# Kernel optimization log

Hardware: AMD Instinct MI355X
Metric: run time of the kernel (lower is better)

## Reference

```python
import jax, jax.numpy as jnp
import numpy as np

U = 512  # units

def hard_sigmoid(x):
    # Keras hard_sigmoid: clip(0.2*x + 0.5, 0, 1)
    return jnp.clip(0.2 * x + 0.5, 0.0, 1.0)

def setup_inputs() -> dict:
    key = jax.random.key(0)
    ks = jax.random.split(key, 9)
    B, T, A, D = 64, 2048, 512, 512  # batch, annotation steps, annotation units, input dim
    s = lambda k, shape, scale: jax.random.normal(k, shape, jnp.float32) * scale
    return {
        "inputs": s(ks[0], (B, D), 1.0),
        "h": s(ks[1], (B, U), 1.0),
        "c": s(ks[2], (B, U), 1.0),
        "annotations": s(ks[3], (B, T, A), 1.0),
        "kernel": s(ks[4], (D + A, 4 * U), 0.02),
        "recurrent_kernel": s(ks[5], (U, 4 * U), 0.02),
        "bias": jnp.zeros((6 * U,), jnp.float32).at[U:2 * U].set(1.0),  # unit_forget_bias
        "kernel_u": s(ks[6], (A, U), 0.02),
        "kernel_w": s(ks[7], (U, U), 0.02),
        "kernel_v": s(ks[8], (U,), 0.02),
    }

def reference(inputs, h, c, annotations, kernel, recurrent_kernel, bias, kernel_u, kernel_w, kernel_v):
    bias_u = bias[4 * U:5 * U]
    # precomputed annotation projection (done once in build()): [B,T,U]
    uh = jnp.einsum('bta,au->btu', annotations, kernel_u) + bias_u
    # Bahdanau attention scores
    Wxstm = h @ kernel_w                                   # [B,U]
    et = jnp.einsum('btu,u->bt', jnp.tanh(uh + Wxstm[:, None, :]), kernel_v)
    at = jax.nn.softmax(et, axis=1)                        # exp/sum in source == softmax
    context = jnp.einsum('bt,bta->ba', at, annotations)    # [B,A]
    x = jnp.concatenate([inputs, context], axis=-1)        # [B, D+A]
    z = x @ kernel + h @ recurrent_kernel + bias[:4 * U]   # [B,4U]
    i = hard_sigmoid(z[:, :U])
    f = hard_sigmoid(z[:, U:2 * U])
    c_new = f * c + i * jnp.tanh(z[:, 2 * U:3 * U])
    o = hard_sigmoid(z[:, 3 * U:])
    h_new = o * jnp.tanh(c_new)
    return h_new
```

## Files before the change

### kernel.cpp

```cpp
#include <hip/hip_runtime.h>

constexpr int U = 512;
constexpr int B = 64;
constexpr int T = 2048;
constexpr int A = 512;

typedef __attribute__((ext_vector_type(8))) short short8;
typedef __attribute__((ext_vector_type(4))) float f32x4;

__device__ __forceinline__ unsigned short f32_to_bf16(float f) {
    unsigned int b = __float_as_uint(f);
    unsigned int r = (b + 0x7FFFu + ((b >> 16) & 1u)) >> 16;
    return (unsigned short)r;
}

__device__ __forceinline__ float bf16_to_f32(short s) {
    return __uint_as_float(((unsigned int)(unsigned short)s) << 16);
}

__device__ __forceinline__ float fast_tanh(float x) {
    float e = exp2f(x * 2.885390081777927f);
    return (e - 1.0f) * __builtin_amdgcn_rcpf(e + 1.0f);
}

__device__ __forceinline__ float hard_sigmoid(float z) {
    return fminf(fmaxf(0.2f * z + 0.5f, 0.0f), 1.0f);
}

__global__ __launch_bounds__(256) void k_prep_s(const float* __restrict__ h,
                                                const float* __restrict__ kw,
                                                float* __restrict__ Sp) {
    int b = blockIdx.x >> 2;
    int kc = blockIdx.x & 3;
    int u = threadIdx.x;
    const float* hb = h + b * U + kc * 128;
    const float* kwb = kw + (size_t)kc * 128 * U;
    float a0 = 0.f, a1 = 0.f;
#pragma unroll 4
    for (int k = 0; k < 128; ++k) {
        float hv = hb[k];
        a0 += hv * kwb[(size_t)k * U + u];
        a1 += hv * kwb[(size_t)k * U + u + 256];
    }
    float* p = Sp + ((size_t)kc * 64 + b) * U;
    p[u] = a0;
    p[u + 256] = a1;
}

__global__ __launch_bounds__(256) void k_s_reduce(const float* __restrict__ Sp,
                                                  const float* __restrict__ bias,
                                                  float* __restrict__ S) {
    int gid = blockIdx.x * 256 + threadIdx.x;
    int b = gid >> 9, u = gid & 511;
    float s = bias[4 * U + u];
#pragma unroll
    for (int kc = 0; kc < 4; ++kc) s += Sp[((size_t)kc * 64 + b) * U + u];
    S[gid] = s;
}

__global__ __launch_bounds__(256) void k_prep_kut(const float* __restrict__ ku,
                                                  unsigned short* __restrict__ kut) {
    __shared__ float tile[32][33];
    int a0 = (blockIdx.x >> 4) << 5;
    int u0 = (blockIdx.x & 15) << 5;
    int c = threadIdx.x & 31, r0 = threadIdx.x >> 5;
#pragma unroll
    for (int p = 0; p < 4; ++p) {
        int r = r0 + p * 8;
        tile[r][c] = ku[(a0 + r) * U + u0 + c];
    }
    __syncthreads();
#pragma unroll
    for (int p = 0; p < 4; ++p) {
        int r = r0 + p * 8;
        kut[(u0 + r) * A + a0 + c] = f32_to_bf16(tile[c][r]);
    }
}

__global__ __launch_bounds__(256) void k_prep_wt(const float* __restrict__ kern,
                                                 const float* __restrict__ rk,
                                                 unsigned short* __restrict__ Wt) {
    __shared__ float tile[32][33];
    int k0 = blockIdx.x << 5;
    int j0 = blockIdx.y << 5;
    int c = threadIdx.x & 31, r0 = threadIdx.x >> 5;
#pragma unroll
    for (int p = 0; p < 4; ++p) {
        int r = r0 + p * 8;
        int k = k0 + r;
        float val = (k < 1024) ? kern[k * 2048 + j0 + c]
                               : rk[(k - 1024) * 2048 + j0 + c];
        tile[r][c] = val;
    }
    __syncthreads();
#pragma unroll
    for (int p = 0; p < 4; ++p) {
        int r = r0 + p * 8;
        Wt[(size_t)(j0 + r) * 1536 + k0 + c] = f32_to_bf16(tile[c][r]);
    }
}

__global__ __launch_bounds__(256, 2) void k_gemm_et(const float* __restrict__ ann,
                                                    const unsigned short* __restrict__ kut,
                                                    const float* __restrict__ S,
                                                    const float* __restrict__ v,
                                                    unsigned short* __restrict__ annb,
                                                    float* __restrict__ etp) {
    __shared__ unsigned short As[128 * 64];
    __shared__ unsigned short Bs[256 * 64];
    __shared__ float red[4][64];

    const int tid = threadIdx.x;
    const int wave = tid >> 6;
    const int lane = tid & 63;
    const int lanelo = lane & 15;
    const int quad = lane >> 4;
    const int wm = wave >> 1, wn = wave & 1;

    const int bid = blockIdx.x;
    const int nt = (bid >> 3) & 1;
    const int mt = (bid & 7) | ((bid >> 4) << 3);
    const int b = mt >> 4;
    const float* aBase = ann + (size_t)mt * 128 * A;
    const unsigned short* bBase = kut + (size_t)nt * 256 * A;
    unsigned short* abOut = annb + (size_t)mt * 128 * A;

    f32x4 acc[4][8];
#pragma unroll
    for (int i = 0; i < 4; ++i)
#pragma unroll
        for (int j = 0; j < 8; ++j) acc[i][j] = {0.f, 0.f, 0.f, 0.f};

    for (int k0 = 0; k0 < A; k0 += 64) {
#pragma unroll
        for (int p = 0; p < 8; ++p) {
            int seg = p * 4 + wave;
            int flat = seg * 1024 + lane * 16;
            int row = flat >> 7;
            int sc = (flat >> 4) & 7;
            int d = sc ^ (row & 7);
            __builtin_amdgcn_global_load_lds(
                (const __attribute__((address_space(1))) void*)(bBase + (size_t)row * A + k0 + d * 8),
                (__attribute__((address_space(3))) void*)((char*)Bs + seg * 1024),
                16, 0, 0);
        }
#pragma unroll
        for (int p = 0; p < 4; ++p) {
            int flat8 = p * 256 + tid;
            int row = flat8 >> 3;
            int c8 = flat8 & 7;
            const float* src = aBase + (size_t)row * A + k0 + c8 * 8;
            f32x4 v0 = *(const f32x4*)src;
            f32x4 v1 = *(const f32x4*)(src + 4);
            short8 pk;
            pk[0] = (short)f32_to_bf16(v0.x);
            pk[1] = (short)f32_to_bf16(v0.y);
            pk[2] = (short)f32_to_bf16(v0.z);
            pk[3] = (short)f32_to_bf16(v0.w);
            pk[4] = (short)f32_to_bf16(v1.x);
            pk[5] = (short)f32_to_bf16(v1.y);
            pk[6] = (short)f32_to_bf16(v1.z);
            pk[7] = (short)f32_to_bf16(v1.w);
            *(short8*)&As[row * 64 + ((c8 ^ (row & 7)) * 8)] = pk;
            if (nt == 0)
                *(short8*)(abOut + (size_t)row * A + k0 + c8 * 8) = pk;
        }
        __syncthreads();
#pragma unroll
        for (int s = 0; s < 2; ++s) {
            int c = s * 4 + quad;
            short8 af[4];
#pragma unroll
            for (int mi = 0; mi < 4; ++mi) {
                int row = wm * 64 + mi * 16 + lanelo;
                af[mi] = *(const short8*)&As[row * 64 + ((c ^ (row & 7)) * 8)];
            }
            short8 bfr[8];
#pragma unroll
            for (int ni = 0; ni < 8; ++ni) {
                int rowb = wn * 128 + ni * 16 + lanelo;
                bfr[ni] = *(const short8*)&Bs[rowb * 64 + ((c ^ (rowb & 7)) * 8)];
            }
#pragma unroll
            for (int mi = 0; mi < 4; ++mi)
#pragma unroll
                for (int ni = 0; ni < 8; ++ni)
                    acc[mi][ni] = __builtin_amdgcn_mfma_f32_16x16x32_bf16(
                        af[mi], bfr[ni], acc[mi][ni], 0, 0, 0);
        }
        __syncthreads();
    }

    float rows[16];
#pragma unroll
    for (int i = 0; i < 16; ++i) rows[i] = 0.f;
#pragma unroll
    for (int ni = 0; ni < 8; ++ni) {
        int n = nt * 256 + wn * 128 + ni * 16 + lanelo;
        float sv = S[b * U + n];
        float vv = v[n];
#pragma unroll
        for (int mi = 0; mi < 4; ++mi)
#pragma unroll
            for (int r = 0; r < 4; ++r)
                rows[mi * 4 + r] += fast_tanh(acc[mi][ni][r] + sv) * vv;
    }
#pragma unroll
    for (int i = 0; i < 16; ++i) {
        rows[i] += __shfl_xor(rows[i], 1);
        rows[i] += __shfl_xor(rows[i], 2);
        rows[i] += __shfl_xor(rows[i], 4);
        rows[i] += __shfl_xor(rows[i], 8);
    }
    if (lanelo == 0) {
#pragma unroll
        for (int mi = 0; mi < 4; ++mi)
#pragma unroll
            for (int r = 0; r < 4; ++r)
                red[wave][mi * 16 + quad * 4 + r] = rows[mi * 4 + r];
    }
    __syncthreads();
    if (tid < 128) {
        int wmv = tid >> 6, ml = tid & 63;
        float sum = red[wmv * 2][ml] + red[wmv * 2 + 1][ml];
        etp[(size_t)nt * (1024 * 128) + (size_t)mt * 128 + tid] = sum;
    }
}

__global__ __launch_bounds__(256) void k_softmax(const float* __restrict__ etp,
                                                 float* __restrict__ at) {
    __shared__ float sred[256];
    int b = blockIdx.x;
    const float* e = etp + b * T;
    float vals[8];
    float mx = -1e30f;
#pragma unroll
    for (int i = 0; i < 8; ++i) {
        int t = threadIdx.x + i * 256;
        float x = e[t] + e[131072 + t];
        vals[i] = x;
        mx = fmaxf(mx, x);
    }
    sred[threadIdx.x] = mx;
    __syncthreads();
    for (int s = 128; s > 0; s >>= 1) {
        if (threadIdx.x < s) sred[threadIdx.x] = fmaxf(sred[threadIdx.x], sred[threadIdx.x + s]);
        __syncthreads();
    }
    mx = sred[0];
    __syncthreads();
    float sum = 0.f;
#pragma unroll
    for (int i = 0; i < 8; ++i) {
        float x = exp2f((vals[i] - mx) * 1.4426950408889634f);
        vals[i] = x;
        sum += x;
    }
    sred[threadIdx.x] = sum;
    __syncthreads();
    for (int s = 128; s > 0; s >>= 1) {
        if (threadIdx.x < s) sred[threadIdx.x] += sred[threadIdx.x + s];
        __syncthreads();
    }
    float inv = 1.0f / sred[0];
#pragma unroll
    for (int i = 0; i < 8; ++i) at[b * T + threadIdx.x + i * 256] = vals[i] * inv;
}

__global__ __launch_bounds__(256) void k_ctx_part(const float* __restrict__ at,
                                                  const unsigned short* __restrict__ annb,
                                                  float* __restrict__ part) {
    __shared__ float buf[4][512];
    int b = blockIdx.x >> 3;
    int tc = blockIdx.x & 7;
    int wave = threadIdx.x >> 6;
    int lane = threadIdx.x & 63;
    const unsigned short* ab = annb + ((size_t)b * T + tc * 256) * A + lane * 8;
    const float* atb = at + b * T + tc * 256;
    float acc[8];
#pragma unroll
    for (int i = 0; i < 8; ++i) acc[i] = 0.f;
    for (int t = wave; t < 256; t += 4) {
        float w = atb[t];
        short8 rv = *(const short8*)(ab + (size_t)t * A);
#pragma unroll
        for (int i = 0; i < 8; ++i) acc[i] += w * bf16_to_f32(rv[i]);
    }
#pragma unroll
    for (int i = 0; i < 8; ++i) buf[wave][lane * 8 + i] = acc[i];
    __syncthreads();
    int a2 = threadIdx.x << 1;
    float s0 = buf[0][a2] + buf[1][a2] + buf[2][a2] + buf[3][a2];
    float s1 = buf[0][a2 + 1] + buf[1][a2 + 1] + buf[2][a2 + 1] + buf[3][a2 + 1];
    float* p = part + ((size_t)b * 8 + tc) * A;
    p[a2] = s0;
    p[a2 + 1] = s1;
}

__global__ __launch_bounds__(256) void k_ctx_reduce(const float* __restrict__ part,
                                                    float* __restrict__ ctx) {
    int b = blockIdx.x;
    for (int a = threadIdx.x; a < A; a += 256) {
        float s = 0.f;
#pragma unroll
        for (int c = 0; c < 8; ++c) s += part[((size_t)b * 8 + c) * A + a];
        ctx[b * A + a] = s;
    }
}

__global__ __launch_bounds__(256) void k_prep_xb(const float* __restrict__ inputs,
                                                 const float* __restrict__ ctx,
                                                 const float* __restrict__ h,
                                                 unsigned short* __restrict__ xb) {
    int b = blockIdx.y;
    int k = blockIdx.x * 256 + threadIdx.x;
    float val;
    if (k < 512) val = inputs[b * 512 + k];
    else if (k < 1024) val = ctx[b * 512 + (k - 512)];
    else val = h[b * 512 + (k - 1024)];
    xb[b * 1536 + k] = f32_to_bf16(val);
}

__global__ __launch_bounds__(256) void k_zgemm(const unsigned short* __restrict__ xb,
                                               const unsigned short* __restrict__ Wt,
                                               float* __restrict__ zpart) {
    const int kc = blockIdx.x & 7;
    const int nt = blockIdx.x >> 3;
    const int wave = threadIdx.x >> 6;
    const int lane = threadIdx.x & 63;
    const int lanelo = lane & 15;
    const int quad = lane >> 4;

    const int n = nt * 64 + wave * 16 + lanelo;
    const unsigned short* bp = Wt + (size_t)n * 1536 + kc * 192 + quad * 8;
    const unsigned short* ap = xb + (size_t)lanelo * 1536 + kc * 192 + quad * 8;

    f32x4 acc[4];
#pragma unroll
    for (int i = 0; i < 4; ++i) acc[i] = {0.f, 0.f, 0.f, 0.f};

#pragma unroll
    for (int ks = 0; ks < 6; ++ks) {
        short8 bfrag = *(const short8*)(bp + ks * 32);
#pragma unroll
        for (int mi = 0; mi < 4; ++mi) {
            short8 afrag = *(const short8*)(ap + (size_t)mi * 16 * 1536 + ks * 32);
            acc[mi] = __builtin_amdgcn_mfma_f32_16x16x32_bf16(afrag, bfrag, acc[mi], 0, 0, 0);
        }
    }

    float* p = zpart + (size_t)kc * 64 * 2048;
#pragma unroll
    for (int mi = 0; mi < 4; ++mi)
#pragma unroll
        for (int r = 0; r < 4; ++r) {
            int m = mi * 16 + quad * 4 + r;
            p[(size_t)m * 2048 + n] = acc[mi][r];
        }
}

__global__ __launch_bounds__(256) void k_gates(const float* __restrict__ zpart,
                                               const float* __restrict__ bias,
                                               const float* __restrict__ c,
                                               float* __restrict__ hnew) {
    int gid = blockIdx.x * 256 + threadIdx.x;
    int b = gid >> 9;
    int u = gid & 511;
    float z[4];
#pragma unroll
    for (int g = 0; g < 4; ++g) {
        int j = (g << 9) + u;
        float s = bias[j];
#pragma unroll
        for (int kc = 0; kc < 8; ++kc)
            s += zpart[((size_t)kc * 64 + b) * 2048 + j];
        z[g] = s;
    }
    float ig = hard_sigmoid(z[0]);
    float fg = hard_sigmoid(z[1]);
    float cn = fg * c[b * 512 + u] + ig * fast_tanh(z[2]);
    float og = hard_sigmoid(z[3]);
    hnew[b * 512 + u] = og * fast_tanh(cn);
}

extern "C" void kernel_launch(void* const* d_in, const int* in_sizes, int n_in,
                              void* d_out, int out_size, void* d_ws, size_t ws_size,
                              hipStream_t stream) {
    const float* inputs = (const float*)d_in[0];
    const float* h      = (const float*)d_in[1];
    const float* c      = (const float*)d_in[2];
    const float* ann    = (const float*)d_in[3];
    const float* kern   = (const float*)d_in[4];
    const float* rk     = (const float*)d_in[5];
    const float* bias   = (const float*)d_in[6];
    const float* ku     = (const float*)d_in[7];
    const float* kw     = (const float*)d_in[8];
    const float* kv     = (const float*)d_in[9];

    char* ws = (char*)d_ws;
    float*          S     = (float*)(ws + 0);
    unsigned short* kut   = (unsigned short*)(ws + 131072);
    float*          etp   = (float*)(ws + 655360);
    float*          at    = (float*)(ws + 1703936);
    float*          part  = (float*)(ws + 2228224);
    float*          Sp    = (float*)(ws + 2228224);
    float*          ctx   = (float*)(ws + 3276800);
    unsigned short* xb    = (unsigned short*)(ws + 3407872);
    unsigned short* Wt    = (unsigned short*)(ws + 3604480);
    float*          zpart = (float*)(ws + 9895936);
    unsigned short* annb  = (unsigned short*)(ws + 16777216);
    float*          hnew  = (float*)d_out;

    k_prep_wt<<<dim3(48, 64), 256, 0, stream>>>(kern, rk, Wt);
    k_prep_kut<<<256, 256, 0, stream>>>(ku, kut);
    k_prep_s<<<256, 256, 0, stream>>>(h, kw, Sp);
    k_s_reduce<<<128, 256, 0, stream>>>(Sp, bias, S);
    k_gemm_et<<<2048, 256, 0, stream>>>(ann, kut, S, kv, annb, etp);
    k_softmax<<<64, 256, 0, stream>>>(etp, at);
    k_ctx_part<<<64 * 8, 256, 0, stream>>>(at, annb, part);
    k_ctx_reduce<<<64, 256, 0, stream>>>(part, ctx);
    k_prep_xb<<<dim3(6, 64), 256, 0, stream>>>(inputs, ctx, h, xb);
    k_zgemm<<<256, 256, 0, stream>>>(xb, Wt, zpart);
    k_gates<<<128, 256, 0, stream>>>(zpart, bias, c, hnew);
}
```

Measured before the change: 558.6 us.

## Split annotation bf16 conversion into separate kernel and DMA A tiles to LDS

Moves the fp32-to-bf16 conversion of the annotations out of the attention GEMM into a standalone grid-stride kernel. The GEMM then loads bf16 A tiles straight into LDS with global_load_lds, like the B tiles, and its occupancy hint rises to 3 blocks per CU. Before, the GEMM read the fp32 annotations twice (once per N-tile) and converted them in registers. Now they are read once in fp32, written once in bf16, and read twice in bf16. The cost is an extra kernel launch and an extra bf16 write and read pass over a large tensor.

```diff
diff --git a/kernel.cpp b/kernel.cpp
--- a/kernel.cpp
+++ b/kernel.cpp
@@ -25,6 +25,27 @@
 
 __device__ __forceinline__ float hard_sigmoid(float z) {
     return fminf(fmaxf(0.2f * z + 0.5f, 0.0f), 1.0f);
+}
+
+__global__ __launch_bounds__(256) void k_convert(const float* __restrict__ ann,
+                                                 unsigned short* __restrict__ annb) {
+    const size_t nchunks = (size_t)B * T * A / 8;
+    const size_t stride = (size_t)gridDim.x * blockDim.x;
+    for (size_t c = (size_t)blockIdx.x * blockDim.x + threadIdx.x; c < nchunks; c += stride) {
+        const float* src = ann + c * 8;
+        f32x4 v0 = *(const f32x4*)src;
+        f32x4 v1 = *(const f32x4*)(src + 4);
+        short8 pk;
+        pk[0] = (short)f32_to_bf16(v0.x);
+        pk[1] = (short)f32_to_bf16(v0.y);
+        pk[2] = (short)f32_to_bf16(v0.z);
+        pk[3] = (short)f32_to_bf16(v0.w);
+        pk[4] = (short)f32_to_bf16(v1.x);
+        pk[5] = (short)f32_to_bf16(v1.y);
+        pk[6] = (short)f32_to_bf16(v1.z);
+        pk[7] = (short)f32_to_bf16(v1.w);
+        *(short8*)(annb + c * 8) = pk;
+    }
 }
 
 __global__ __launch_bounds__(256) void k_prep_s(const float* __restrict__ h,
@@ -100,11 +121,10 @@
     }
 }
 
-__global__ __launch_bounds__(256, 2) void k_gemm_et(const float* __restrict__ ann,
+__global__ __launch_bounds__(256, 3) void k_gemm_et(const unsigned short* __restrict__ annb,
                                                     const unsigned short* __restrict__ kut,
                                                     const float* __restrict__ S,
                                                     const float* __restrict__ v,
-                                                    unsigned short* __restrict__ annb,
                                                     float* __restrict__ etp) {
     __shared__ unsigned short As[128 * 64];
     __shared__ unsigned short Bs[256 * 64];
@@ -121,9 +141,8 @@
     const int nt = (bid >> 3) & 1;
     const int mt = (bid & 7) | ((bid >> 4) << 3);
     const int b = mt >> 4;
-    const float* aBase = ann + (size_t)mt * 128 * A;
+    const unsigned short* aBase = annb + (size_t)mt * 128 * A;
     const unsigned short* bBase = kut + (size_t)nt * 256 * A;
-    unsigned short* abOut = annb + (size_t)mt * 128 * A;
 
     f32x4 acc[4][8];
 #pragma unroll
@@ -146,24 +165,15 @@
         }
 #pragma unroll
         for (int p = 0; p < 4; ++p) {
-            int flat8 = p * 256 + tid;
-            int row = flat8 >> 3;
-            int c8 = flat8 & 7;
-            const float* src = aBase + (size_t)row * A + k0 + c8 * 8;
-            f32x4 v0 = *(const f32x4*)src;
-            f32x4 v1 = *(const f32x4*)(src + 4);
-            short8 pk;
-            pk[0] = (short)f32_to_bf16(v0.x);
-            pk[1] = (short)f32_to_bf16(v0.y);
-            pk[2] = (short)f32_to_bf16(v0.z);
-            pk[3] = (short)f32_to_bf16(v0.w);
-            pk[4] = (short)f32_to_bf16(v1.x);
-            pk[5] = (short)f32_to_bf16(v1.y);
-            pk[6] = (short)f32_to_bf16(v1.z);
-            pk[7] = (short)f32_to_bf16(v1.w);
-            *(short8*)&As[row * 64 + ((c8 ^ (row & 7)) * 8)] = pk;
-            if (nt == 0)
-                *(short8*)(abOut + (size_t)row * A + k0 + c8 * 8) = pk;
+            int seg = p * 4 + wave;
+            int flat = seg * 1024 + lane * 16;
+            int row = flat >> 7;
+            int sc = (flat >> 4) & 7;
+            int d = sc ^ (row & 7);
+            __builtin_amdgcn_global_load_lds(
+                (const __attribute__((address_space(1))) void*)(aBase + (size_t)row * A + k0 + d * 8),
+                (__attribute__((address_space(3))) void*)((char*)As + seg * 1024),
+                16, 0, 0);
         }
         __syncthreads();
 #pragma unroll
@@ -411,11 +421,12 @@
     unsigned short* annb  = (unsigned short*)(ws + 16777216);
     float*          hnew  = (float*)d_out;
 
+    k_convert<<<2048, 256, 0, stream>>>(ann, annb);
     k_prep_wt<<<dim3(48, 64), 256, 0, stream>>>(kern, rk, Wt);
     k_prep_kut<<<256, 256, 0, stream>>>(ku, kut);
     k_prep_s<<<256, 256, 0, stream>>>(h, kw, Sp);
     k_s_reduce<<<128, 256, 0, stream>>>(Sp, bias, S);
-    k_gemm_et<<<2048, 256, 0, stream>>>(ann, kut, S, kv, annb, etp);
+    k_gemm_et<<<2048, 256, 0, stream>>>(annb, kut, S, kv, etp);
     k_softmax<<<64, 256, 0, stream>>>(etp, at);
     k_ctx_part<<<64 * 8, 256, 0, stream>>>(at, annb, part);
     k_ctx_reduce<<<64, 256, 0, stream>>>(part, ctx);
```

Measured after the change: 691.5 us. 23.8% more time.
